# Kernel tuning notes

Measured on AMD Instinct MI355X. Metric: run time of the kernel, lower is better.

The kernel has to match this reference:

```python
import jax, jax.numpy as jnp
import numpy as np

D_MODEL = 1024
NUM_HEADS = 16
D_HEAD = D_MODEL // NUM_HEADS
NEG_BIG = 10000000000.0  # matches the torch module's -1e10 mask constant


def setup_inputs() -> dict:
    key = jax.random.key(0)
    ks = jax.random.split(key, 9)
    d = D_MODEL
    scale = 1.0 / np.sqrt(d)
    inp = {
        "x": jax.random.normal(ks[0], (2, 2048, d), dtype=jnp.float32),
        "W_q": jax.random.normal(ks[1], (d, d), dtype=jnp.float32) * scale,
        "b_q": jnp.zeros((d,), dtype=jnp.float32),
        "W_k": jax.random.normal(ks[2], (d, d), dtype=jnp.float32) * scale,
        "b_k": jnp.zeros((d,), dtype=jnp.float32),
        "W_v": jax.random.normal(ks[3], (d, d), dtype=jnp.float32) * scale,
        "b_v": jnp.zeros((d,), dtype=jnp.float32),
        "W_o": jax.random.normal(ks[4], (d, d), dtype=jnp.float32) * scale,
        "b_o": jnp.zeros((d,), dtype=jnp.float32),
    }
    return inp


def reference(x, W_q, b_q, W_k, b_k, W_v, b_v, W_o, b_o):
    B, S, d = x.shape
    H, Dh = NUM_HEADS, D_HEAD

    Q = x @ W_q + b_q  # [B,S,d]
    K = x @ W_k + b_k
    V = x @ W_v + b_v

    # split heads: [B,S,d] -> [B,H,S,Dh]
    Qh = Q.reshape(B, S, H, Dh).transpose(0, 2, 1, 3)
    Kh = K.reshape(B, S, H, Dh).transpose(0, 2, 1, 3)
    Vh = V.reshape(B, S, H, Dh).transpose(0, 2, 1, 3)

    scores = jnp.einsum("bhid,bhjd->bhij", Qh, Kh) / jnp.sqrt(
        jnp.asarray(Dh, dtype=x.dtype)
    )

    # causal mask: tril(scores) - 1e10 * (1 - tril_mask)
    causal = jnp.tril(jnp.ones((S, S), dtype=x.dtype))
    scores = scores * causal - NEG_BIG * (1.0 - causal)

    attn = jax.nn.softmax(scores, axis=-1)  # dropout p=0.0 -> identity

    vals = jnp.einsum("bhij,bhjd->bhid", attn, Vh)  # [B,H,S,Dh]
    vals = vals.transpose(0, 2, 1, 3).reshape(B, S, d)

    return vals @ W_o + b_o
```

## Files before the change

kernel.cpp:

```cpp
#include <hip/hip_runtime.h>

typedef unsigned short u16;
typedef __attribute__((ext_vector_type(8))) short short8;
typedef __attribute__((ext_vector_type(4))) short shortx4;
typedef __attribute__((ext_vector_type(4))) float floatx4;

#define S_ 2048
#define D_ 1024
#define DQKV_ 3072
#define H_ 16
#define DH_ 64

#define EXP2F(x) __builtin_amdgcn_exp2f(x)

__device__ __forceinline__ float bf2f(u16 x) {
    union { unsigned int u; float f; } v; v.u = ((unsigned int)x) << 16; return v.f;
}
__device__ __forceinline__ u16 f2bf(float f) {
    unsigned int u = __float_as_uint(f);
    return (u16)((u + 0x7fffu + ((u >> 16) & 1u)) >> 16);
}
__device__ __forceinline__ u16 f2bf_fast(float f) {
    return (u16)((__float_as_uint(f) + 0x8000u) >> 16);
}

__device__ __forceinline__ void async16(const void* g, void* l) {
    __builtin_amdgcn_global_load_lds(
        (const __attribute__((address_space(1))) unsigned int*)g,
        (__attribute__((address_space(3))) unsigned int*)l, 16, 0, 0);
}

__global__ __launch_bounds__(256) void convert_x(const float* __restrict__ x, u16* __restrict__ xb) {
    const size_t i = ((size_t)blockIdx.x * 256 + threadIdx.x) * 4;
    float4 v = *(const float4*)&x[i];
    shortx4 h;
    h[0] = (short)f2bf(v.x); h[1] = (short)f2bf(v.y);
    h[2] = (short)f2bf(v.z); h[3] = (short)f2bf(v.w);
    *(shortx4*)&xb[i] = h;
}

__global__ __launch_bounds__(256) void transpose_w4(const float* __restrict__ Wq, const float* __restrict__ Wk,
                                                    const float* __restrict__ Wv, const float* __restrict__ Wo,
                                                    u16* __restrict__ Wqkvt, u16* __restrict__ Wot) {
    __shared__ u16 tile[32][33];
    const int z = blockIdx.z;
    const float* W = (z == 0) ? Wq : (z == 1) ? Wk : (z == 2) ? Wv : Wo;
    u16* dst = (z == 3) ? Wot : (Wqkvt + (size_t)z * D_ * D_);
    const int tx = threadIdx.x, ty = threadIdx.y;
    const int n0 = blockIdx.x * 32, k0 = blockIdx.y * 32;
#pragma unroll
    for (int r = 0; r < 4; ++r) {
        int k = ty + r * 8;
        tile[k][tx] = f2bf(W[(size_t)(k0 + k) * D_ + n0 + tx]);
    }
    __syncthreads();
#pragma unroll
    for (int r = 0; r < 4; ++r) {
        int n = ty + r * 8;
        dst[(size_t)(n0 + n) * D_ + k0 + tx] = tile[tx][n];
    }
}

__global__ __launch_bounds__(256) void transpose_headV(const u16* __restrict__ QKV, u16* __restrict__ Vt) {
    __shared__ u16 tile[64 * 65];
    const int t = threadIdx.x;
    const int bh = blockIdx.y, b = bh >> 4, h = bh & 15;
    const int s0 = blockIdx.x << 6;
#pragma unroll
    for (int i = 0; i < 16; ++i) {
        int idx = t + (i << 8);
        int s = idx >> 6, d = idx & 63;
        tile[s * 65 + d] = QKV[(size_t)(b * S_ + s0 + s) * DQKV_ + 2048 + h * DH_ + d];
    }
    __syncthreads();
#pragma unroll
    for (int i = 0; i < 16; ++i) {
        int idx = t + (i << 8);
        int d = idx >> 6, s = idx & 63;
        Vt[((size_t)bh * DH_ + d) * S_ + s0 + s] = tile[s * 65 + d];
    }
}

template <int BM, int BN, bool OUTF32>
__global__ __launch_bounds__(256) void gemm_bt(const u16* __restrict__ A, const u16* __restrict__ Bt,
                                               const float* __restrict__ b0, const float* __restrict__ b1,
                                               const float* __restrict__ b2, void* __restrict__ Cp,
                                               int M, int N, int Kd) {
    constexpr int FI = BM / 32, FJ = BN / 32;
    __shared__ __align__(16) u16 As[BM * 32];
    __shared__ __align__(16) u16 Bs[BN * 32];
    const int t = threadIdx.x;
    const int m0 = blockIdx.y * BM, n0 = blockIdx.x * BN;
    const int w = t >> 6, lane = t & 63;
    const int lr = lane & 15, lg = lane >> 4;
    const int wm = (w >> 1) * (BM / 2), wn = (w & 1) * (BN / 2);
    const int srow = lane >> 2, scol = (lane & 3) << 3;
    floatx4 acc[FI][FJ] = {};

    for (int k0 = 0; k0 < Kd; k0 += 32) {
#pragma unroll
        for (int c = 0; c < BM / 64; ++c) {
            int rbase = (w * (BM / 64) + c) * 16;
            async16(&A[(size_t)(m0 + rbase + srow) * Kd + k0 + scol], &As[rbase * 32]);
        }
#pragma unroll
        for (int c = 0; c < BN / 64; ++c) {
            int rbase = (w * (BN / 64) + c) * 16;
            async16(&Bt[(size_t)(n0 + rbase + srow) * Kd + k0 + scol], &Bs[rbase * 32]);
        }
        __syncthreads();
        short8 af[FI], bfr[FJ];
#pragma unroll
        for (int i = 0; i < FI; ++i) af[i]  = *(const short8*)&As[(wm + i * 16 + lr) * 32 + lg * 8];
#pragma unroll
        for (int j = 0; j < FJ; ++j) bfr[j] = *(const short8*)&Bs[(wn + j * 16 + lr) * 32 + lg * 8];
#pragma unroll
        for (int i = 0; i < FI; ++i)
#pragma unroll
            for (int j = 0; j < FJ; ++j)
                acc[i][j] = __builtin_amdgcn_mfma_f32_16x16x32_bf16(af[i], bfr[j], acc[i][j], 0, 0, 0);
        __syncthreads();
    }

#pragma unroll
    for (int j = 0; j < FJ; ++j) {
        int col = n0 + wn + j * 16 + lr;
        const float* bp = (col < 1024) ? b0 : (col < 2048) ? b1 : b2;
        float bv = bp[col & 1023];
#pragma unroll
        for (int i = 0; i < FI; ++i) {
            int rb = m0 + wm + i * 16 + lg * 4;
#pragma unroll
            for (int ii = 0; ii < 4; ++ii) {
                float val = acc[i][j][ii] + bv;
                if (OUTF32) ((float*)Cp)[(size_t)(rb + ii) * N + col] = val;
                else        ((u16*)Cp)[(size_t)(rb + ii) * N + col] = f2bf(val);
            }
        }
    }
}

__global__ __launch_bounds__(256) void attn_mfma(const u16* __restrict__ QKV, const u16* __restrict__ Vt,
                                                 u16* __restrict__ O) {
    __shared__ __align__(16) u16 KsA[2][64 * 64];
    __shared__ __align__(16) u16 VsA[2][64 * 64];
    __shared__ __align__(16) u16 Ps[4 * 16 * 76];
    const int t = threadIdx.x, w = t >> 6, lane = t & 63;
    const int lr = lane & 15, lg = lane >> 4;
    const int bh = blockIdx.x, b = bh >> 4, h = bh & 15;
    const int qt = 31 - blockIdx.y;
    const int q0 = qt << 6;
    const float cs = 0.18033688f;

    const u16* Kb  = QKV + (size_t)b * S_ * DQKV_ + 1024 + h * DH_;
    const u16* Vtb = Vt + (size_t)bh * DH_ * S_;
    u16* Pw = Ps + w * (16 * 76);

    const int rb = lane >> 3;
    const int cc = ((lane & 7) ^ rb) << 3;
    const int swz = lr & 7;

    short8 qf[2];
#pragma unroll
    for (int ks = 0; ks < 2; ++ks)
        qf[ks] = *(const short8*)&QKV[(size_t)(b * S_ + q0 + w * 16 + lr) * DQKV_ + h * DH_ + ks * 32 + lg * 8];

    floatx4 of[4] = {};
    float lsum[4] = {0.f, 0.f, 0.f, 0.f};

    {
        u16* Kd = &KsA[0][w * 512];
        u16* Vd = &VsA[0][w * 512];
        async16(&Kb[(size_t)(w * 8 + rb) * DQKV_ + cc], Kd);
        async16(&Kb[(size_t)(32 + w * 8 + rb) * DQKV_ + cc], Kd + 2048);
        async16(&Vtb[(size_t)(w * 8 + rb) * S_ + cc], Vd);
        async16(&Vtb[(size_t)(32 + w * 8 + rb) * S_ + cc], Vd + 2048);
    }

    for (int kb = 0; kb <= qt; ++kb) {
        const int cur = kb & 1;
        __syncthreads();
        if (kb < qt) {
            const int K1 = (kb + 1) << 6;
            u16* Kd = &KsA[cur ^ 1][w * 512];
            u16* Vd = &VsA[cur ^ 1][w * 512];
            async16(&Kb[(size_t)(K1 + w * 8 + rb) * DQKV_ + cc], Kd);
            async16(&Kb[(size_t)(K1 + 32 + w * 8 + rb) * DQKV_ + cc], Kd + 2048);
            async16(&Vtb[(size_t)(w * 8 + rb) * S_ + K1 + cc], Vd);
            async16(&Vtb[(size_t)(32 + w * 8 + rb) * S_ + K1 + cc], Vd + 2048);
        }
        const u16* Kc = KsA[cur];
        const u16* Vc = VsA[cur];

        floatx4 sf[4] = {};
#pragma unroll
        for (int ks = 0; ks < 2; ++ks)
#pragma unroll
            for (int j = 0; j < 4; ++j) {
                short8 kf = *(const short8*)&Kc[(j * 16 + lr) * 64 + ((((ks << 2) + lg) ^ swz) << 3)];
                sf[j] = __builtin_amdgcn_mfma_f32_16x16x32_bf16(qf[ks], kf, sf[j], 0, 0, 0);
            }

        const bool diag = (kb == qt);
#pragma unroll
        for (int j = 0; j < 4; ++j)
#pragma unroll
            for (int ii = 0; ii < 4; ++ii) {
                float ev = EXP2F(sf[j][ii] * cs);
                if (diag && (j * 16 + lr > w * 16 + lg * 4 + ii)) ev = 0.f;
                lsum[ii] += ev;
                Pw[(lg * 4 + ii) * 76 + j * 16 + lr] = f2bf_fast(ev);
            }

#pragma unroll
        for (int ks = 0; ks < 2; ++ks) {
            union { short8 v; shortx4 hh[2]; } pa;
            pa.hh[0] = *(const shortx4*)&Pw[lr * 76 + ks * 32 + lg * 8];
            pa.hh[1] = *(const shortx4*)&Pw[lr * 76 + ks * 32 + lg * 8 + 4];
#pragma unroll
            for (int j = 0; j < 4; ++j) {
                short8 vf = *(const short8*)&Vc[(j * 16 + lr) * 64 + ((((ks << 2) + lg) ^ swz) << 3)];
                of[j] = __builtin_amdgcn_mfma_f32_16x16x32_bf16(pa.v, vf, of[j], 0, 0, 0);
            }
        }
    }

    float rinv[4];
#pragma unroll
    for (int ii = 0; ii < 4; ++ii) {
        float s = lsum[ii];
#pragma unroll
        for (int off = 1; off < 16; off <<= 1) s += __shfl_xor(s, off);
        rinv[ii] = 1.f / s;
    }
#pragma unroll
    for (int j = 0; j < 4; ++j)
#pragma unroll
        for (int ii = 0; ii < 4; ++ii)
            O[(size_t)(b * S_ + q0 + w * 16 + lg * 4 + ii) * D_ + h * DH_ + j * 16 + lr] =
                f2bf(of[j][ii] * rinv[ii]);
}

extern "C" void kernel_launch(void* const* d_in, const int* in_sizes, int n_in,
                              void* d_out, int out_size, void* d_ws, size_t ws_size,
                              hipStream_t stream) {
    (void)in_sizes; (void)n_in; (void)out_size; (void)ws_size;
    const float* x  = (const float*)d_in[0];
    const float* Wq = (const float*)d_in[1];
    const float* bq = (const float*)d_in[2];
    const float* Wk = (const float*)d_in[3];
    const float* bk = (const float*)d_in[4];
    const float* Wv = (const float*)d_in[5];
    const float* bv = (const float*)d_in[6];
    const float* Wo = (const float*)d_in[7];
    const float* bo = (const float*)d_in[8];

    u16* ws    = (u16*)d_ws;
    u16* WqkvT = ws;
    u16* WoT   = ws + (size_t)3 * (1 << 20);
    u16* QKV   = ws + (size_t)4 * (1 << 20);
    u16* Vtm   = ws + (size_t)16 * (1 << 20);
    u16* xbf   = ws + (size_t)20 * (1 << 20);
    u16* Am    = ws + (size_t)20 * (1 << 20);

    convert_x<<<4096, 256, 0, stream>>>(x, xbf);
    transpose_w4<<<dim3(32, 32, 4), dim3(32, 8), 0, stream>>>(Wq, Wk, Wv, Wo, WqkvT, WoT);

    gemm_bt<128, 128, false><<<dim3(DQKV_ / 128, 4096 / 128), 256, 0, stream>>>(
        xbf, WqkvT, bq, bk, bv, QKV, 4096, DQKV_, 1024);

    transpose_headV<<<dim3(32, 32), 256, 0, stream>>>(QKV, Vtm);

    attn_mfma<<<dim3(32, 32), 256, 0, stream>>>(QKV, Vtm, Am);

    gemm_bt<64, 128, true><<<dim3(1024 / 128, 4096 / 64), 256, 0, stream>>>(
        Am, WoT, bo, bo, bo, d_out, 4096, 1024, 1024);
}
```

Before: 194.5 us.

## Double-buffer GEMM shared tiles and swizzle attention P buffer for vector reads

```diff
diff --git a/kernel.cpp b/kernel.cpp
--- a/kernel.cpp
+++ b/kernel.cpp
@@ -87,8 +87,8 @@
                                                const float* __restrict__ b2, void* __restrict__ Cp,
                                                int M, int N, int Kd) {
     constexpr int FI = BM / 32, FJ = BN / 32;
-    __shared__ __align__(16) u16 As[BM * 32];
-    __shared__ __align__(16) u16 Bs[BN * 32];
+    __shared__ __align__(16) u16 As[2][BM * 32];
+    __shared__ __align__(16) u16 Bs[2][BN * 32];
     const int t = threadIdx.x;
     const int m0 = blockIdx.y * BM, n0 = blockIdx.x * BN;
     const int w = t >> 6, lane = t & 63;
@@ -97,29 +97,36 @@
     const int srow = lane >> 2, scol = (lane & 3) << 3;
     floatx4 acc[FI][FJ] = {};
 
-    for (int k0 = 0; k0 < Kd; k0 += 32) {
+    auto stage = [&](int buf, int k0) {
 #pragma unroll
         for (int c = 0; c < BM / 64; ++c) {
             int rbase = (w * (BM / 64) + c) * 16;
-            async16(&A[(size_t)(m0 + rbase + srow) * Kd + k0 + scol], &As[rbase * 32]);
+            async16(&A[(size_t)(m0 + rbase + srow) * Kd + k0 + scol], &As[buf][rbase * 32]);
         }
 #pragma unroll
         for (int c = 0; c < BN / 64; ++c) {
             int rbase = (w * (BN / 64) + c) * 16;
-            async16(&Bt[(size_t)(n0 + rbase + srow) * Kd + k0 + scol], &Bs[rbase * 32]);
-        }
+            async16(&Bt[(size_t)(n0 + rbase + srow) * Kd + k0 + scol], &Bs[buf][rbase * 32]);
+        }
+    };
+
+    stage(0, 0);
+    const int nk = Kd / 32;
+    for (int kk = 0; kk < nk; ++kk) {
+        const int cur = kk & 1;
         __syncthreads();
+        if (kk + 1 < nk) stage(cur ^ 1, (kk + 1) * 32);
+
         short8 af[FI], bfr[FJ];
 #pragma unroll
-        for (int i = 0; i < FI; ++i) af[i]  = *(const short8*)&As[(wm + i * 16 + lr) * 32 + lg * 8];
-#pragma unroll
-        for (int j = 0; j < FJ; ++j) bfr[j] = *(const short8*)&Bs[(wn + j * 16 + lr) * 32 + lg * 8];
+        for (int i = 0; i < FI; ++i) af[i]  = *(const short8*)&As[cur][(wm + i * 16 + lr) * 32 + lg * 8];
+#pragma unroll
+        for (int j = 0; j < FJ; ++j) bfr[j] = *(const short8*)&Bs[cur][(wn + j * 16 + lr) * 32 + lg * 8];
 #pragma unroll
         for (int i = 0; i < FI; ++i)
 #pragma unroll
             for (int j = 0; j < FJ; ++j)
                 acc[i][j] = __builtin_amdgcn_mfma_f32_16x16x32_bf16(af[i], bfr[j], acc[i][j], 0, 0, 0);
-        __syncthreads();
     }
 
 #pragma unroll
@@ -144,7 +151,7 @@
                                                  u16* __restrict__ O) {
     __shared__ __align__(16) u16 KsA[2][64 * 64];
     __shared__ __align__(16) u16 VsA[2][64 * 64];
-    __shared__ __align__(16) u16 Ps[4 * 16 * 76];
+    __shared__ __align__(16) u16 Ps[4 * 16 * 64];
     const int t = threadIdx.x, w = t >> 6, lane = t & 63;
     const int lr = lane & 15, lg = lane >> 4;
     const int bh = blockIdx.x, b = bh >> 4, h = bh & 15;
@@ -154,7 +161,7 @@
 
     const u16* Kb  = QKV + (size_t)b * S_ * DQKV_ + 1024 + h * DH_;
     const u16* Vtb = Vt + (size_t)bh * DH_ * S_;
-    u16* Pw = Ps + w * (16 * 76);
+    u16* Pw = Ps + w * (16 * 64);
 
     const int rb = lane >> 3;
     const int cc = ((lane & 7) ^ rb) << 3;
@@ -209,18 +216,18 @@
                 float ev = EXP2F(sf[j][ii] * cs);
                 if (diag && (j * 16 + lr > w * 16 + lg * 4 + ii)) ev = 0.f;
                 lsum[ii] += ev;
-                Pw[(lg * 4 + ii) * 76 + j * 16 + lr] = f2bf_fast(ev);
+                int r = lg * 4 + ii;
+                int chunk = ((j * 2 + (lr >> 3)) ^ (r & 7));
+                Pw[r * 64 + (chunk << 3) + (lr & 7)] = f2bf_fast(ev);
             }
 
 #pragma unroll
         for (int ks = 0; ks < 2; ++ks) {
-            union { short8 v; shortx4 hh[2]; } pa;
-            pa.hh[0] = *(const shortx4*)&Pw[lr * 76 + ks * 32 + lg * 8];
-            pa.hh[1] = *(const shortx4*)&Pw[lr * 76 + ks * 32 + lg * 8 + 4];
+            short8 pa = *(const short8*)&Pw[lr * 64 + ((((ks << 2) + lg) ^ swz) << 3)];
 #pragma unroll
             for (int j = 0; j < 4; ++j) {
                 short8 vf = *(const short8*)&Vc[(j * 16 + lr) * 64 + ((((ks << 2) + lg) ^ swz) << 3)];
-                of[j] = __builtin_amdgcn_mfma_f32_16x16x32_bf16(pa.v, vf, of[j], 0, 0, 0);
+                of[j] = __builtin_amdgcn_mfma_f32_16x16x32_bf16(pa, vf, of[j], 0, 0, 0);
             }
         }
     }
```

Result: no change. 191.0 us (-1.8%).
